# Kernel tuning notes

Measured on AMD Instinct MI355X. Metric: run time of the kernel, lower is better.

The kernel has to match this reference:

```python
import jax, jax.numpy as jnp
import numpy as np

N_NODES = 500_000
N_EDGES = 16_000_000
N_LAYERS = 49
ALPHA = 0.3  # GCN2Conv alpha; beta = 1.0 (no theta/layer given)

# per-layer activation applied AFTER the conv (layer index 0-based)
_LEAKY = {1, 11, 21, 31, 41}
_SIG = {4, 14, 24, 34, 44}


def setup_inputs() -> dict:
    key = jax.random.key(0)
    k1, k2, k3 = jax.random.split(key, 3)
    x = jax.random.normal(k1, (N_NODES, 1), dtype=jnp.float32)
    adj = jax.random.randint(k2, (2, N_EDGES), 0, N_NODES, dtype=jnp.int64)
    # 49 scalar (1x1) layer weights
    w = jax.random.normal(k3, (N_LAYERS,), dtype=jnp.float32) * 0.1
    return {"input": x, "w": w, "adj": adj}


def _gcn_norm(adj, n):
    # add self-loops, symmetric normalization D^-1/2 (A+I) D^-1/2
    loops = jnp.arange(n, dtype=adj.dtype)
    src = jnp.concatenate([adj[0], loops])
    dst = jnp.concatenate([adj[1], loops])
    deg = jax.ops.segment_sum(jnp.ones(src.shape[0], jnp.float32), dst, num_segments=n)
    dis = 1.0 / jnp.sqrt(deg)  # deg >= 1 due to self-loops
    ew = dis[src] * dis[dst]
    return src, dst, ew


def reference(input, w, adj):
    n = input.shape[0]
    x0 = input.astype(jnp.float32)
    src, dst, ew = _gcn_norm(adj, n)
    ewc = ew[:, None]  # [E+N, 1]

    def gcn2(x, wl):
        h = jax.ops.segment_sum(ewc * x[src], dst, num_segments=n)  # A_hat @ x
        comb = (1.0 - ALPHA) * h + ALPHA * x0                       # residual mix
        return comb * wl                                            # 1x1 weight, beta=1

    x = x0
    for i in range(N_LAYERS):
        y = gcn2(x, w[i])
        if i == 0:
            x = y  # no activation after gcn1
        elif i == N_LAYERS - 1:
            x = n * jax.nn.sigmoid(y)  # CustomSigmoid: len(x) * sigmoid(x)
        elif i in _LEAKY:
            x = jax.nn.leaky_relu(y, 0.01)
        elif i in _SIG:
            x = jax.nn.sigmoid(y)
        else:
            x = jax.nn.relu(y)
        # dropout(p=0.0) is identity
    return jnp.squeeze(x, 1).astype(jnp.int64)
```

## Files before the change

kernel.cpp:

```cpp
#include <hip/hip_runtime.h>
#include <math.h>
#include <stdint.h>

#define NN 500000
#define NE 16000000
#define NT 62
#define NQ 8
#define OCTW 62500
#define NCH (NT * NQ)
#define PB 65536
#define NPB ((NE + PB - 1) / PB)
#define CH_CAP 34000
#define ZPAD 524288
#define SENT 0xFFFFFFFFu

__global__ __launch_bounds__(1024) void hist_kernel(const int4* __restrict__ src4,
                                                    const int4* __restrict__ dst4,
                                                    int* __restrict__ bcnt) {
    __shared__ int lh[NCH];
    for (int i = threadIdx.x; i < NCH; i += 1024) lh[i] = 0;
    __syncthreads();
    long base4 = (long)blockIdx.x * (PB / 4);
    for (int k = 0; k < PB / 4; k += 1024) {
        long i4 = base4 + k + threadIdx.x;
        if (i4 < NE / 4) {
            int4 d = dst4[i4];
            int4 s = src4[i4];
            atomicAdd(&lh[(d.x >> 13) * NQ + s.x / OCTW], 1);
            atomicAdd(&lh[(d.y >> 13) * NQ + s.y / OCTW], 1);
            atomicAdd(&lh[(d.z >> 13) * NQ + s.z / OCTW], 1);
            atomicAdd(&lh[(d.w >> 13) * NQ + s.w / OCTW], 1);
        }
    }
    __syncthreads();
    for (int i = threadIdx.x; i < NCH; i += 1024) {
        int c = lh[i];
        if (c) atomicAdd(&bcnt[i], c);
    }
}

__global__ __launch_bounds__(512) void scan_buckets(const int* __restrict__ bcnt,
                                                    int* __restrict__ bbase,
                                                    int* __restrict__ bcur) {
    __shared__ int scn[512];
    __shared__ int tot;
    int i = threadIdx.x;
    int v = (i < NCH) ? bcnt[i] : 0;
    int pv = (v + 15) & ~15;
    scn[i] = pv;
    __syncthreads();
    for (int off = 1; off < 512; off <<= 1) {
        int t = (i >= off) ? scn[i - off] : 0;
        __syncthreads();
        scn[i] += t;
        __syncthreads();
    }
    int excl = scn[i] - pv;
    if (i < NCH) { bbase[i] = excl; bcur[i] = excl; }
    if (i == 511) tot = scn[511];
    __syncthreads();
    if (i == 0) bbase[NCH] = tot;
}

__global__ __launch_bounds__(1024) void partition_kernel(const int4* __restrict__ src4,
                                                         const int4* __restrict__ dst4,
                                                         int* __restrict__ bcur,
                                                         uint32_t* __restrict__ ebuf) {
    __shared__ int lh[NCH];
    for (int i = threadIdx.x; i < NCH; i += 1024) lh[i] = 0;
    __syncthreads();
    long base4 = (long)blockIdx.x * (PB / 4);
    for (int k = 0; k < PB / 4; k += 1024) {
        long i4 = base4 + k + threadIdx.x;
        if (i4 < NE / 4) {
            int4 d = dst4[i4];
            int4 s = src4[i4];
            atomicAdd(&lh[(d.x >> 13) * NQ + s.x / OCTW], 1);
            atomicAdd(&lh[(d.y >> 13) * NQ + s.y / OCTW], 1);
            atomicAdd(&lh[(d.z >> 13) * NQ + s.z / OCTW], 1);
            atomicAdd(&lh[(d.w >> 13) * NQ + s.w / OCTW], 1);
        }
    }
    __syncthreads();
    for (int i = threadIdx.x; i < NCH; i += 1024) {
        int c = lh[i];
        if (c) lh[i] = atomicAdd(&bcur[i], c);
    }
    __syncthreads();
    for (int k = 0; k < PB / 4; k += 1024) {
        long i4 = base4 + k + threadIdx.x;
        if (i4 < NE / 4) {
            int4 d = dst4[i4];
            int4 s = src4[i4];
            int pos;
            pos = atomicAdd(&lh[(d.x >> 13) * NQ + s.x / OCTW], 1);
            ebuf[pos] = ((uint32_t)(d.x & 8191) << 19) | (uint32_t)s.x;
            pos = atomicAdd(&lh[(d.y >> 13) * NQ + s.y / OCTW], 1);
            ebuf[pos] = ((uint32_t)(d.y & 8191) << 19) | (uint32_t)s.y;
            pos = atomicAdd(&lh[(d.z >> 13) * NQ + s.z / OCTW], 1);
            ebuf[pos] = ((uint32_t)(d.z & 8191) << 19) | (uint32_t)s.z;
            pos = atomicAdd(&lh[(d.w >> 13) * NQ + s.w / OCTW], 1);
            ebuf[pos] = ((uint32_t)(d.w & 8191) << 19) | (uint32_t)s.w;
        }
    }
}

__global__ __launch_bounds__(1024) void chunk_sort(const int* __restrict__ bcnt,
                                                   const int* __restrict__ bbase,
                                                   uint32_t* __restrict__ ebuf,
                                                   int* __restrict__ deg) {
    __shared__ uint32_t sorted[CH_CAP];
    __shared__ int ghist[4096];
    __shared__ int scn[1024];
    int c = blockIdx.x;
    int base = bbase[c];
    int pend = bbase[c + 1];
    int n = bcnt[c];
    if (n > CH_CAP) n = CH_CAP;
    int t = c >> 3;
    int octbase = (c & 7) * OCTW;
    int* dh = (int*)sorted;
    for (int i = threadIdx.x; i < 4096; i += 1024) ghist[i] = 0;
    for (int i = threadIdx.x; i < 8192; i += 1024) dh[i] = 0;
    __syncthreads();
    for (int i = threadIdx.x; i < n; i += 1024) {
        uint32_t w = ebuf[base + i];
        int s = (int)(w & 0x7FFFFu);
        atomicAdd(&ghist[(s - octbase) >> 4], 1);
        atomicAdd(&dh[w >> 19], 1);
    }
    __syncthreads();
    for (int i = threadIdx.x; i < 8192; i += 1024) {
        int d = dh[i];
        if (d) atomicAdd(&deg[t * 8192 + i], d);
    }
    __syncthreads();
    int b4 = threadIdx.x * 4;
    int l0 = ghist[b4], l1 = ghist[b4 + 1], l2 = ghist[b4 + 2], l3 = ghist[b4 + 3];
    int ls = l0 + l1 + l2 + l3;
    scn[threadIdx.x] = ls;
    __syncthreads();
    for (int off = 1; off < 1024; off <<= 1) {
        int tv = (threadIdx.x >= off) ? scn[threadIdx.x - off] : 0;
        __syncthreads();
        scn[threadIdx.x] += tv;
        __syncthreads();
    }
    int ex = scn[threadIdx.x] - ls;
    ghist[b4] = ex; ghist[b4 + 1] = ex + l0;
    ghist[b4 + 2] = ex + l0 + l1; ghist[b4 + 3] = ex + l0 + l1 + l2;
    __syncthreads();
    for (int i = threadIdx.x; i < n; i += 1024) {
        uint32_t w = ebuf[base + i];
        int k = ((int)(w & 0x7FFFFu) - octbase) >> 4;
        int pos = atomicAdd(&ghist[k], 1);
        sorted[pos] = w;
    }
    __syncthreads();
    for (int i = threadIdx.x; base + i < pend; i += 1024)
        ebuf[base + i] = (i < n) ? sorted[i] : SENT;
}

__global__ void dis_kernel(const int* __restrict__ deg, const float* __restrict__ x0,
                           float* __restrict__ dis, float* __restrict__ z0) {
    int v = blockIdx.x * 512 + threadIdx.x;
    if (v < NN) {
        float d = rsqrtf((float)(deg[v] + 1));
        dis[v] = d;
        z0[v] = x0[v] * d;
    }
}

__global__ __launch_bounds__(1024) void scatter_kernel(const int* __restrict__ bbase,
                                                       const uint32_t* __restrict__ ebuf,
                                                       const float* __restrict__ zin,
                                                       float* __restrict__ hp) {
    __shared__ float acc[8192];
    int c = blockIdx.x;
    for (int i = threadIdx.x; i < 8192; i += 1024) acc[i] = 0.f;
    __syncthreads();
    int b4 = bbase[c] >> 2, e4 = bbase[c + 1] >> 2;
    const uint4* __restrict__ eb4 = (const uint4*)ebuf;
    for (int i4 = b4 + threadIdx.x; i4 < e4; i4 += 1024) {
        uint4 w = eb4[i4];
        float a0 = zin[w.x & 0x7FFFFu];
        float a1 = zin[w.y & 0x7FFFFu];
        float a2 = zin[w.z & 0x7FFFFu];
        float a3 = zin[w.w & 0x7FFFFu];
        atomicAdd(&acc[w.x >> 19], a0);
        atomicAdd(&acc[w.y >> 19], a1);
        atomicAdd(&acc[w.z >> 19], a2);
        atomicAdd(&acc[w.w >> 19], a3);
    }
    __syncthreads();
    int t = c >> 3, q = c & 7;
    float* dstp = hp + (size_t)q * (NT * 8192) + t * 8192;
    for (int k = threadIdx.x; k < 8192; k += 1024) dstp[k] = acc[k];
}

__global__ __launch_bounds__(512) void combine_kernel(const float4* __restrict__ hp4,
        const float4* __restrict__ zin4, const float4* __restrict__ dis4,
        const float4* __restrict__ x04, const float* __restrict__ w,
        int li, int act, float4* __restrict__ zout4, int4* __restrict__ out4) {
    int v4 = blockIdx.x * 512 + threadIdx.x;
    if (v4 >= NN / 4) return;
    float4 s = zin4[v4];
    #pragma unroll
    for (int q = 0; q < NQ; q++) {
        float4 hq = hp4[(size_t)q * (NT * 8192 / 4) + v4];
        s.x += hq.x; s.y += hq.y; s.z += hq.z; s.w += hq.w;
    }
    float4 dv = dis4[v4];
    float4 xv = x04[v4];
    float wl = w[li];
    float y0 = (0.7f * dv.x * s.x + 0.3f * xv.x) * wl;
    float y1 = (0.7f * dv.y * s.y + 0.3f * xv.y) * wl;
    float y2 = (0.7f * dv.z * s.z + 0.3f * xv.z) * wl;
    float y3 = (0.7f * dv.w * s.w + 0.3f * xv.w) * wl;
    if (act == 4) {
        int4 o;
        o.x = (int)(500000.f / (1.f + expf(-y0)));
        o.y = (int)(500000.f / (1.f + expf(-y1)));
        o.z = (int)(500000.f / (1.f + expf(-y2)));
        o.w = (int)(500000.f / (1.f + expf(-y3)));
        out4[v4] = o;
        return;
    }
    float r0, r1, r2, r3;
    if (act == 0)      { r0 = y0; r1 = y1; r2 = y2; r3 = y3; }
    else if (act == 1) { r0 = fmaxf(y0, 0.f); r1 = fmaxf(y1, 0.f);
                         r2 = fmaxf(y2, 0.f); r3 = fmaxf(y3, 0.f); }
    else if (act == 2) { r0 = (y0 > 0.f) ? y0 : 0.01f * y0;
                         r1 = (y1 > 0.f) ? y1 : 0.01f * y1;
                         r2 = (y2 > 0.f) ? y2 : 0.01f * y2;
                         r3 = (y3 > 0.f) ? y3 : 0.01f * y3; }
    else               { r0 = 1.f / (1.f + expf(-y0)); r1 = 1.f / (1.f + expf(-y1));
                         r2 = 1.f / (1.f + expf(-y2)); r3 = 1.f / (1.f + expf(-y3)); }
    float4 zo;
    zo.x = dv.x * r0; zo.y = dv.y * r1; zo.z = dv.z * r2; zo.w = dv.w * r3;
    zout4[v4] = zo;
}

extern "C" void kernel_launch(void* const* d_in, const int* in_sizes, int n_in,
                              void* d_out, int out_size, void* d_ws, size_t ws_size,
                              hipStream_t stream) {
    const float* x0  = (const float*)d_in[0];
    const float* w   = (const float*)d_in[1];
    const int*   adj = (const int*)d_in[2];
    const int*   src = adj;
    const int*   dst = adj + NE;
    int* out = (int*)d_out;

    uintptr_t p = (uintptr_t)d_ws;
    auto alloc = [&](size_t bytes) -> void* {
        p = (p + 255) & ~(uintptr_t)255;
        void* r = (void*)p;
        p += bytes;
        return r;
    };
    float* dis   = (float*)alloc((size_t)NN * 4);
    float* z0    = (float*)alloc((size_t)ZPAD * 4);
    float* z1    = (float*)alloc((size_t)ZPAD * 4);
    int*   bcnt  = (int*)alloc((size_t)NCH * 4);
    int*   bbase = (int*)alloc((size_t)(NCH + 1) * 4);
    int*   bcur  = (int*)alloc((size_t)NCH * 4);
    uint32_t* csr = (uint32_t*)alloc(((size_t)NE + 8192) * 4);
    float* hp    = (float*)alloc((size_t)NQ * NT * 8192 * 4);
    int*   deg   = (int*)hp;
    (void)ws_size;

    hipMemsetAsync(bcnt, 0, (size_t)NCH * 4, stream);
    hipMemsetAsync(deg, 0, (size_t)NT * 8192 * 4, stream);
    hipMemsetAsync(z0, 0, (size_t)ZPAD * 4, stream);
    hipMemsetAsync(z1, 0, (size_t)ZPAD * 4, stream);

    hist_kernel<<<NPB, 1024, 0, stream>>>((const int4*)src, (const int4*)dst, bcnt);
    scan_buckets<<<1, 512, 0, stream>>>(bcnt, bbase, bcur);
    partition_kernel<<<NPB, 1024, 0, stream>>>((const int4*)src, (const int4*)dst, bcur, csr);
    chunk_sort<<<NCH, 1024, 0, stream>>>(bcnt, bbase, csr, deg);
    dis_kernel<<<(NN + 511) / 512, 512, 0, stream>>>(deg, x0, dis, z0);

    float* zbuf[2] = {z0, z1};
    const int CB = (NN / 4 + 511) / 512;
    for (int i = 0; i < 49; i++) {
        int act;
        if (i == 0)            act = 0;
        else if (i == 48)      act = 4;
        else if (i % 10 == 1)  act = 2;
        else if (i % 10 == 4)  act = 3;
        else                   act = 1;
        scatter_kernel<<<NCH, 1024, 0, stream>>>(bbase, csr, zbuf[i & 1], hp);
        combine_kernel<<<CB, 512, 0, stream>>>((const float4*)hp, (const float4*)zbuf[i & 1],
                                               (const float4*)dis, (const float4*)x0, w,
                                               i, act, (float4*)zbuf[(i + 1) & 1], (int4*)out);
    }
}
```

Measured before the change: 4.935 ms.

## Stage source tiles in LDS for scatter and use fixed-slot edge buckets

Edge buckets now sit in fixed-size slots per chunk, so the separate histogram and scan passes are dropped and partitioning becomes a single pass. The chunk sort repacks each edge with a 16-bit source offset and records sub-range bases. The per-layer scatter then loads each 8192-wide slice of the source vector into shared memory and gathers from LDS instead of random global reads. The trade-offs are a larger edge buffer, a less coalesced per-element edge load in place of uint4 loads, and eight extra barriers per layer per block.

```diff
diff --git a/kernel.cpp b/kernel.cpp
--- a/kernel.cpp
+++ b/kernel.cpp
@@ -11,12 +11,12 @@
 #define PB 65536
 #define NPB ((NE + PB - 1) / PB)
 #define CH_CAP 34000
-#define ZPAD 524288
-#define SENT 0xFFFFFFFFu
-
-__global__ __launch_bounds__(1024) void hist_kernel(const int4* __restrict__ src4,
-                                                    const int4* __restrict__ dst4,
-                                                    int* __restrict__ bcnt) {
+#define SLOT 34048
+
+__global__ __launch_bounds__(1024) void partition_kernel(const int4* __restrict__ src4,
+                                                         const int4* __restrict__ dst4,
+                                                         int* __restrict__ bcnt,
+                                                         uint32_t* __restrict__ ebuf) {
     __shared__ int lh[NCH];
     for (int i = threadIdx.x; i < NCH; i += 1024) lh[i] = 0;
     __syncthreads();
@@ -35,86 +35,36 @@
     __syncthreads();
     for (int i = threadIdx.x; i < NCH; i += 1024) {
         int c = lh[i];
-        if (c) atomicAdd(&bcnt[i], c);
-    }
-}
-
-__global__ __launch_bounds__(512) void scan_buckets(const int* __restrict__ bcnt,
-                                                    int* __restrict__ bbase,
-                                                    int* __restrict__ bcur) {
-    __shared__ int scn[512];
-    __shared__ int tot;
-    int i = threadIdx.x;
-    int v = (i < NCH) ? bcnt[i] : 0;
-    int pv = (v + 15) & ~15;
-    scn[i] = pv;
-    __syncthreads();
-    for (int off = 1; off < 512; off <<= 1) {
-        int t = (i >= off) ? scn[i - off] : 0;
-        __syncthreads();
-        scn[i] += t;
-        __syncthreads();
-    }
-    int excl = scn[i] - pv;
-    if (i < NCH) { bbase[i] = excl; bcur[i] = excl; }
-    if (i == 511) tot = scn[511];
-    __syncthreads();
-    if (i == 0) bbase[NCH] = tot;
-}
-
-__global__ __launch_bounds__(1024) void partition_kernel(const int4* __restrict__ src4,
-                                                         const int4* __restrict__ dst4,
-                                                         int* __restrict__ bcur,
-                                                         uint32_t* __restrict__ ebuf) {
-    __shared__ int lh[NCH];
-    for (int i = threadIdx.x; i < NCH; i += 1024) lh[i] = 0;
-    __syncthreads();
-    long base4 = (long)blockIdx.x * (PB / 4);
+        if (c) lh[i] = atomicAdd(&bcnt[i], c);
+    }
+    __syncthreads();
     for (int k = 0; k < PB / 4; k += 1024) {
         long i4 = base4 + k + threadIdx.x;
         if (i4 < NE / 4) {
             int4 d = dst4[i4];
             int4 s = src4[i4];
-            atomicAdd(&lh[(d.x >> 13) * NQ + s.x / OCTW], 1);
-            atomicAdd(&lh[(d.y >> 13) * NQ + s.y / OCTW], 1);
-            atomicAdd(&lh[(d.z >> 13) * NQ + s.z / OCTW], 1);
-            atomicAdd(&lh[(d.w >> 13) * NQ + s.w / OCTW], 1);
+            int ch, rel;
+            ch = (d.x >> 13) * NQ + s.x / OCTW; rel = atomicAdd(&lh[ch], 1);
+            if (rel < CH_CAP) ebuf[(size_t)ch * SLOT + rel] = ((uint32_t)(d.x & 8191) << 19) | (uint32_t)s.x;
+            ch = (d.y >> 13) * NQ + s.y / OCTW; rel = atomicAdd(&lh[ch], 1);
+            if (rel < CH_CAP) ebuf[(size_t)ch * SLOT + rel] = ((uint32_t)(d.y & 8191) << 19) | (uint32_t)s.y;
+            ch = (d.z >> 13) * NQ + s.z / OCTW; rel = atomicAdd(&lh[ch], 1);
+            if (rel < CH_CAP) ebuf[(size_t)ch * SLOT + rel] = ((uint32_t)(d.z & 8191) << 19) | (uint32_t)s.z;
+            ch = (d.w >> 13) * NQ + s.w / OCTW; rel = atomicAdd(&lh[ch], 1);
+            if (rel < CH_CAP) ebuf[(size_t)ch * SLOT + rel] = ((uint32_t)(d.w & 8191) << 19) | (uint32_t)s.w;
         }
     }
-    __syncthreads();
-    for (int i = threadIdx.x; i < NCH; i += 1024) {
-        int c = lh[i];
-        if (c) lh[i] = atomicAdd(&bcur[i], c);
-    }
-    __syncthreads();
-    for (int k = 0; k < PB / 4; k += 1024) {
-        long i4 = base4 + k + threadIdx.x;
-        if (i4 < NE / 4) {
-            int4 d = dst4[i4];
-            int4 s = src4[i4];
-            int pos;
-            pos = atomicAdd(&lh[(d.x >> 13) * NQ + s.x / OCTW], 1);
-            ebuf[pos] = ((uint32_t)(d.x & 8191) << 19) | (uint32_t)s.x;
-            pos = atomicAdd(&lh[(d.y >> 13) * NQ + s.y / OCTW], 1);
-            ebuf[pos] = ((uint32_t)(d.y & 8191) << 19) | (uint32_t)s.y;
-            pos = atomicAdd(&lh[(d.z >> 13) * NQ + s.z / OCTW], 1);
-            ebuf[pos] = ((uint32_t)(d.z & 8191) << 19) | (uint32_t)s.z;
-            pos = atomicAdd(&lh[(d.w >> 13) * NQ + s.w / OCTW], 1);
-            ebuf[pos] = ((uint32_t)(d.w & 8191) << 19) | (uint32_t)s.w;
-        }
-    }
-}
-
-__global__ __launch_bounds__(1024) void chunk_sort(const int* __restrict__ bcnt,
-                                                   const int* __restrict__ bbase,
+}
+
+__global__ __launch_bounds__(1024) void chunk_sort(int* __restrict__ bcnt,
                                                    uint32_t* __restrict__ ebuf,
-                                                   int* __restrict__ deg) {
+                                                   int* __restrict__ deg,
+                                                   int* __restrict__ sbase) {
     __shared__ uint32_t sorted[CH_CAP];
     __shared__ int ghist[4096];
     __shared__ int scn[1024];
     int c = blockIdx.x;
-    int base = bbase[c];
-    int pend = bbase[c + 1];
+    long base = (long)c * SLOT;
     int n = bcnt[c];
     if (n > CH_CAP) n = CH_CAP;
     int t = c >> 3;
@@ -149,16 +99,17 @@
     int ex = scn[threadIdx.x] - ls;
     ghist[b4] = ex; ghist[b4 + 1] = ex + l0;
     ghist[b4 + 2] = ex + l0 + l1; ghist[b4 + 3] = ex + l0 + l1 + l2;
+    if ((threadIdx.x & 127) == 0) sbase[c * 8 + (threadIdx.x >> 7)] = ex;
     __syncthreads();
     for (int i = threadIdx.x; i < n; i += 1024) {
         uint32_t w = ebuf[base + i];
-        int k = ((int)(w & 0x7FFFFu) - octbase) >> 4;
-        int pos = atomicAdd(&ghist[k], 1);
-        sorted[pos] = w;
-    }
-    __syncthreads();
-    for (int i = threadIdx.x; base + i < pend; i += 1024)
-        ebuf[base + i] = (i < n) ? sorted[i] : SENT;
+        int slo = (int)(w & 0x7FFFFu) - octbase;
+        int pos = atomicAdd(&ghist[slo >> 4], 1);
+        sorted[pos] = ((w >> 19) << 16) | (uint32_t)slo;
+    }
+    __syncthreads();
+    for (int i = threadIdx.x; i < n; i += 1024) ebuf[base + i] = sorted[i];
+    if (threadIdx.x == 0) bcnt[c] = n;
 }
 
 __global__ void dis_kernel(const int* __restrict__ deg, const float* __restrict__ x0,
@@ -171,29 +122,36 @@
     }
 }
 
-__global__ __launch_bounds__(1024) void scatter_kernel(const int* __restrict__ bbase,
+__global__ __launch_bounds__(1024) void scatter_kernel(const int* __restrict__ bcnt,
+                                                       const int* __restrict__ sbase,
                                                        const uint32_t* __restrict__ ebuf,
                                                        const float* __restrict__ zin,
                                                        float* __restrict__ hp) {
     __shared__ float acc[8192];
+    __shared__ float ztile[8192];
     int c = blockIdx.x;
     for (int i = threadIdx.x; i < 8192; i += 1024) acc[i] = 0.f;
-    __syncthreads();
-    int b4 = bbase[c] >> 2, e4 = bbase[c + 1] >> 2;
-    const uint4* __restrict__ eb4 = (const uint4*)ebuf;
-    for (int i4 = b4 + threadIdx.x; i4 < e4; i4 += 1024) {
-        uint4 w = eb4[i4];
-        float a0 = zin[w.x & 0x7FFFFu];
-        float a1 = zin[w.y & 0x7FFFFu];
-        float a2 = zin[w.z & 0x7FFFFu];
-        float a3 = zin[w.w & 0x7FFFFu];
-        atomicAdd(&acc[w.x >> 19], a0);
-        atomicAdd(&acc[w.y >> 19], a1);
-        atomicAdd(&acc[w.z >> 19], a2);
-        atomicAdd(&acc[w.w >> 19], a3);
-    }
-    __syncthreads();
+    long base = (long)c * SLOT;
+    int n = bcnt[c];
     int t = c >> 3, q = c & 7;
+    int octbase = q * OCTW;
+    const float4* __restrict__ zin4 = (const float4*)zin;
+    for (int k = 0; k < 8; k++) {
+        int lo = sbase[c * 8 + k];
+        int hi = (k < 7) ? sbase[c * 8 + k + 1] : n;
+        int zoff = k << 13;
+        int zcnt = min(8192, OCTW - zoff);
+        __syncthreads();
+        int zb4 = (octbase + zoff) >> 2;
+        float4* zt4 = (float4*)ztile;
+        for (int j = threadIdx.x; j < (zcnt >> 2); j += 1024) zt4[j] = zin4[zb4 + j];
+        __syncthreads();
+        for (int i = lo + threadIdx.x; i < hi; i += 1024) {
+            uint32_t w = ebuf[base + i];
+            atomicAdd(&acc[w >> 16], ztile[(int)(w & 0xFFFFu) - zoff]);
+        }
+    }
+    __syncthreads();
     float* dstp = hp + (size_t)q * (NT * 8192) + t * 8192;
     for (int k = threadIdx.x; k < 8192; k += 1024) dstp[k] = acc[k];
 }
@@ -259,25 +217,20 @@
         return r;
     };
     float* dis   = (float*)alloc((size_t)NN * 4);
-    float* z0    = (float*)alloc((size_t)ZPAD * 4);
-    float* z1    = (float*)alloc((size_t)ZPAD * 4);
+    float* z0    = (float*)alloc((size_t)NN * 4);
+    float* z1    = (float*)alloc((size_t)NN * 4);
     int*   bcnt  = (int*)alloc((size_t)NCH * 4);
-    int*   bbase = (int*)alloc((size_t)(NCH + 1) * 4);
-    int*   bcur  = (int*)alloc((size_t)NCH * 4);
-    uint32_t* csr = (uint32_t*)alloc(((size_t)NE + 8192) * 4);
+    int*   sbase = (int*)alloc((size_t)NCH * 8 * 4);
+    uint32_t* csr = (uint32_t*)alloc((size_t)NCH * SLOT * 4);
     float* hp    = (float*)alloc((size_t)NQ * NT * 8192 * 4);
     int*   deg   = (int*)hp;
     (void)ws_size;
 
     hipMemsetAsync(bcnt, 0, (size_t)NCH * 4, stream);
     hipMemsetAsync(deg, 0, (size_t)NT * 8192 * 4, stream);
-    hipMemsetAsync(z0, 0, (size_t)ZPAD * 4, stream);
-    hipMemsetAsync(z1, 0, (size_t)ZPAD * 4, stream);
-
-    hist_kernel<<<NPB, 1024, 0, stream>>>((const int4*)src, (const int4*)dst, bcnt);
-    scan_buckets<<<1, 512, 0, stream>>>(bcnt, bbase, bcur);
-    partition_kernel<<<NPB, 1024, 0, stream>>>((const int4*)src, (const int4*)dst, bcur, csr);
-    chunk_sort<<<NCH, 1024, 0, stream>>>(bcnt, bbase, csr, deg);
+
+    partition_kernel<<<NPB, 1024, 0, stream>>>((const int4*)src, (const int4*)dst, bcnt, csr);
+    chunk_sort<<<NCH, 1024, 0, stream>>>(bcnt, csr, deg, sbase);
     dis_kernel<<<(NN + 511) / 512, 512, 0, stream>>>(deg, x0, dis, z0);
 
     float* zbuf[2] = {z0, z1};
@@ -289,7 +242,7 @@
         else if (i % 10 == 1)  act = 2;
         else if (i % 10 == 4)  act = 3;
         else                   act = 1;
-        scatter_kernel<<<NCH, 1024, 0, stream>>>(bbase, csr, zbuf[i & 1], hp);
+        scatter_kernel<<<NCH, 1024, 0, stream>>>(bcnt, sbase, csr, zbuf[i & 1], hp);
         combine_kernel<<<CB, 512, 0, stream>>>((const float4*)hp, (const float4*)zbuf[i & 1],
                                                (const float4*)dis, (const float4*)x0, w,
                                                i, act, (float4*)zbuf[(i + 1) & 1], (int4*)out);
```

Result: slower. 5.242 ms (+6.2%).
